# Optimization experiments

Hardware: AMD Instinct MI355X
Metric: run time of the kernel (lower is better)

Reference implementation:

```python
import jax, jax.numpy as jnp
import numpy as np

B, S, H = 1, 4096, 2048
NH, HD = 16, 128
ROPE_N = 32
WINDOW = 1024
EPS = 1e-5


def _build_rope(seq_len, n_elem, base=10000.0):
    theta = 1.0 / (base ** (np.arange(0, n_elem, 2, dtype=np.float32) / n_elem))  # [n_elem/2]
    idx = np.arange(seq_len, dtype=np.float32)
    freqs = np.outer(idx, theta)                     # [S, n_elem/2]
    freqs = np.concatenate([freqs, freqs], axis=-1)  # [S, n_elem]
    return jnp.asarray(np.cos(freqs)), jnp.asarray(np.sin(freqs))


def setup_inputs() -> dict:
    key = jax.random.key(0)
    k1, k2, k3 = jax.random.split(key, 3)
    x = jax.random.normal(k1, (B, S, H), dtype=jnp.float32)
    cos, sin = _build_rope(S, ROPE_N)
    norm_weight = jnp.ones((H,), dtype=jnp.float32)
    qkv_w = jax.random.normal(k2, (3 * H, H), dtype=jnp.float32) * (1.0 / np.sqrt(H))
    o_w = jax.random.normal(k3, (H, H), dtype=jnp.float32) * (1.0 / np.sqrt(H))
    return {"x": x, "cos": cos, "sin": sin, "norm_weight": norm_weight,
            "qkv_w": qkv_w, "o_w": o_w}


def _apply_rope(t, cos, sin):
    # t: [B, NH, S, ROPE_N]; cos/sin: [S, ROPE_N]
    half = t.shape[-1] // 2
    x1, x2 = t[..., :half], t[..., half:]
    rotated = jnp.concatenate([-x2, x1], axis=-1)
    return t * cos + rotated * sin


def reference(x, cos, sin, norm_weight, qkv_w, o_w):
    b, s, h = x.shape
    # RMSNorm (computed in fp32)
    xf = x.astype(jnp.float32)
    ms = jnp.mean(xf * xf, axis=-1, keepdims=True)
    xn = (norm_weight * (xf * jax.lax.rsqrt(ms + EPS))).astype(x.dtype)
    # fused QKV projection
    qkv = jnp.einsum('bsh,oh->bso', xn, qkv_w)  # [B, S, 3H]
    q, k, v = jnp.split(qkv, 3, axis=-1)
    def to_heads(t):
        return t.reshape(b, s, NH, HD).transpose(0, 2, 1, 3)  # [B, NH, S, HD]
    q, k, v = to_heads(q), to_heads(k), to_heads(v)
    # partial RoPE on first ROPE_N dims
    q = jnp.concatenate([_apply_rope(q[..., :ROPE_N], cos, sin), q[..., ROPE_N:]], axis=-1)
    k = jnp.concatenate([_apply_rope(k[..., :ROPE_N], cos, sin), k[..., ROPE_N:]], axis=-1)
    # sliding-window causal attention: query i attends keys j with i-WINDOW <= j <= i
    scale = 1.0 / np.sqrt(HD)
    scores = jnp.einsum('bnqd,bnkd->bnqk', q, k) * scale  # [B, NH, S, S]
    i = jnp.arange(s)[:, None]
    j = jnp.arange(s)[None, :]
    mask = (j <= i) & (j >= i - WINDOW)
    scores = jnp.where(mask, scores, jnp.finfo(scores.dtype).min)
    attn = jax.nn.softmax(scores, axis=-1)
    out = jnp.einsum('bnqk,bnkd->bnqd', attn, v)  # [B, NH, S, HD]
    out = out.transpose(0, 2, 1, 3).reshape(b, s, h)
    return jnp.einsum('bsh,oh->bso', out, o_w)
```

## Files before the change

kernel.cpp:

```cpp
#include <hip/hip_runtime.h>
#include <stdint.h>

#define S_LEN 4096
#define HDIM  2048
#define NHEAD 16
#define HD    128
#define WIN   1024

typedef float  f32x4  __attribute__((ext_vector_type(4)));
typedef float  f32x4v __attribute__((ext_vector_type(4)));
typedef __bf16 bf16x8 __attribute__((ext_vector_type(8)));
typedef short  short8 __attribute__((ext_vector_type(8)));
typedef short  short4v __attribute__((ext_vector_type(4)));

static __device__ __forceinline__ short f2bf(float f) {
  union { float f; uint32_t u; } v; v.f = f;
  uint32_t r = (v.u + 0x7FFFu + ((v.u >> 16) & 1u)) >> 16;
  return (short)(uint16_t)r;
}

static __device__ __forceinline__ void gload_lds16(const void* g, void* l) {
  __builtin_amdgcn_global_load_lds((__attribute__((address_space(1))) void*)g,
                                   (__attribute__((address_space(3))) void*)l,
                                   16, 0, 0);
}

__global__ __launch_bounds__(256) void rmsnorm_k(const float* __restrict__ x,
                                                 const float* __restrict__ w,
                                                 short* __restrict__ xn) {
  const int row = blockIdx.x;
  const int t = threadIdx.x;
  const float* xr = x + (size_t)row * HDIM;
  f32x4v a = *(const f32x4v*)&xr[t * 8];
  f32x4v b = *(const f32x4v*)&xr[t * 8 + 4];
  float ss = a.x*a.x + a.y*a.y + a.z*a.z + a.w*a.w
           + b.x*b.x + b.y*b.y + b.z*b.z + b.w*b.w;
#pragma unroll
  for (int d = 1; d < 64; d <<= 1) ss += __shfl_xor(ss, d, 64);
  __shared__ float sred[4];
  if ((t & 63) == 0) sred[t >> 6] = ss;
  __syncthreads();
  float tot = sred[0] + sred[1] + sred[2] + sred[3];
  float rs = rsqrtf(tot * (1.0f / HDIM) + 1e-5f);
  float vv[8] = {a.x, a.y, a.z, a.w, b.x, b.y, b.z, b.w};
  const float* wp = w + t * 8;
  short8 o;
#pragma unroll
  for (int j = 0; j < 8; ++j) o[j] = f2bf(vv[j] * rs * wp[j]);
  *(short8*)&xn[(size_t)row * HDIM + t * 8] = o;
}

__global__ __launch_bounds__(256) void cvt_k(const float* __restrict__ in,
                                             short* __restrict__ out, int n4) {
  int i = blockIdx.x * 256 + threadIdx.x;
  if (i >= n4) return;
  f32x4v v = *(const f32x4v*)&in[(size_t)i * 4];
  short4v o = { f2bf(v.x), f2bf(v.y), f2bf(v.z), f2bf(v.w) };
  *(short4v*)&out[(size_t)i * 4] = o;
}

template <int EPI>
__global__ __launch_bounds__(512, 2) void gemm_8p(
    const short* __restrict__ A, const short* __restrict__ Bt,
    int M, int N, int K, float* __restrict__ Cf,
    const float* __restrict__ cosb, const float* __restrict__ sinb,
    short* __restrict__ Qo, short* __restrict__ Ko, short* __restrict__ Vt) {
  __shared__ __align__(16) short lds[2][32768];
  const int t = threadIdx.x;
  const int wid = t >> 6, l = t & 63;
  const int lr = l & 15, lg = l >> 4;
  const int wm = wid >> 2, wn = wid & 3;

  int bid = blockIdx.x;
  const int nwg = gridDim.x;
  bid = (bid & 7) * (nwg >> 3) + (bid >> 3);
  const int nby = M >> 8;
  const int by = bid % nby, bx = bid / nby;
  const int brow = by * 256, bcol = bx * 256;

  const int ssl = ((t & 7) ^ ((t >> 3) & 7)) * 8;
  const short* Asrc = A  + (size_t)(brow + (t >> 3)) * K + ssl;
  const short* Bsrc = Bt + (size_t)(bcol + (t >> 3)) * K + ssl;

#define ST_A0(d, kt) do {                                                \
    gload_lds16(Asrc + (size_t)(kt),            &lds[d][t * 8]);         \
    gload_lds16(Asrc + (size_t)64  * K + (kt),  &lds[d][4096 + t * 8]);  } while (0)
#define ST_A1(d, kt) do {                                                \
    gload_lds16(Asrc + (size_t)128 * K + (kt),  &lds[d][8192 + t * 8]);  \
    gload_lds16(Asrc + (size_t)192 * K + (kt),  &lds[d][12288 + t * 8]); } while (0)
#define ST_B0(d, kt) do {                                                \
    gload_lds16(Bsrc + (size_t)(kt),            &lds[d][16384 + t * 8]); \
    gload_lds16(Bsrc + (size_t)64  * K + (kt),  &lds[d][20480 + t * 8]); } while (0)
#define ST_B1(d, kt) do {                                                \
    gload_lds16(Bsrc + (size_t)128 * K + (kt),  &lds[d][24576 + t * 8]); \
    gload_lds16(Bsrc + (size_t)192 * K + (kt),  &lds[d][28672 + t * 8]); } while (0)

  f32x4 acc[8][4] = {};
  const int nt = K >> 6;

  const int s0 = ((lg     ) ^ (lr & 7)) * 8;
  const int s1 = ((lg + 4) ^ (lr & 7)) * 8;
  const int aB = (wm * 128 + lr) * 64;
  const int bB = 16384 + (wn * 64 + lr) * 64;

  ST_A0(0, 0); ST_A1(0, 0); ST_B0(0, 0); ST_B1(0, 0);
  if (nt > 1) { ST_B0(1, 64); ST_A0(1, 64); ST_A1(1, 64); }
  asm volatile("s_waitcnt vmcnt(6)" ::: "memory");
  __builtin_amdgcn_s_barrier();
  __builtin_amdgcn_sched_barrier(0);

  for (int tt = 0; tt < nt; ++tt) {
    const short* P = &lds[tt & 1][0];
    bf16x8 a03[4][2], a47[4][2], b01[2][2], b23[2][2];

#pragma unroll
    for (int m = 0; m < 4; ++m) {
      a03[m][0] = *(const bf16x8*)&P[aB + m * 1024 + s0];
      a03[m][1] = *(const bf16x8*)&P[aB + m * 1024 + s1];
    }
#pragma unroll
    for (int n = 0; n < 2; ++n) {
      b01[n][0] = *(const bf16x8*)&P[bB + n * 1024 + s0];
      b01[n][1] = *(const bf16x8*)&P[bB + n * 1024 + s1];
    }
    if (tt + 1 < nt) ST_B1((tt & 1) ^ 1, (tt + 1) << 6);
    __builtin_amdgcn_s_setprio(1);
#pragma unroll
    for (int m = 0; m < 4; ++m)
#pragma unroll
      for (int n = 0; n < 2; ++n) {
        acc[m][n] = __builtin_amdgcn_mfma_f32_16x16x32_bf16(a03[m][0], b01[n][0], acc[m][n], 0, 0, 0);
        acc[m][n] = __builtin_amdgcn_mfma_f32_16x16x32_bf16(a03[m][1], b01[n][1], acc[m][n], 0, 0, 0);
      }
    __builtin_amdgcn_s_setprio(0);

#pragma unroll
    for (int n = 0; n < 2; ++n) {
      b23[n][0] = *(const bf16x8*)&P[bB + (n + 2) * 1024 + s0];
      b23[n][1] = *(const bf16x8*)&P[bB + (n + 2) * 1024 + s1];
    }
    __builtin_amdgcn_s_setprio(1);
#pragma unroll
    for (int m = 0; m < 4; ++m)
#pragma unroll
      for (int n = 0; n < 2; ++n) {
        acc[m][n + 2] = __builtin_amdgcn_mfma_f32_16x16x32_bf16(a03[m][0], b23[n][0], acc[m][n + 2], 0, 0, 0);
        acc[m][n + 2] = __builtin_amdgcn_mfma_f32_16x16x32_bf16(a03[m][1], b23[n][1], acc[m][n + 2], 0, 0, 0);
      }
    __builtin_amdgcn_s_setprio(0);

#pragma unroll
    for (int m = 0; m < 4; ++m) {
      a47[m][0] = *(const bf16x8*)&P[aB + (m + 4) * 1024 + s0];
      a47[m][1] = *(const bf16x8*)&P[aB + (m + 4) * 1024 + s1];
    }
    __builtin_amdgcn_s_setprio(1);
#pragma unroll
    for (int m = 0; m < 4; ++m)
#pragma unroll
      for (int n = 0; n < 2; ++n) {
        acc[m + 4][n + 2] = __builtin_amdgcn_mfma_f32_16x16x32_bf16(a47[m][0], b23[n][0], acc[m + 4][n + 2], 0, 0, 0);
        acc[m + 4][n + 2] = __builtin_amdgcn_mfma_f32_16x16x32_bf16(a47[m][1], b23[n][1], acc[m + 4][n + 2], 0, 0, 0);
      }
    __builtin_amdgcn_s_setprio(0);

    asm volatile("" ::: "memory");
    __builtin_amdgcn_s_barrier();
    __builtin_amdgcn_sched_barrier(0);

    if (tt + 2 < nt) {
      const int k2 = (tt + 2) << 6;
      ST_B0(tt & 1, k2); ST_A0(tt & 1, k2); ST_A1(tt & 1, k2);
    }
    __builtin_amdgcn_s_setprio(1);
#pragma unroll
    for (int m = 0; m < 4; ++m)
#pragma unroll
      for (int n = 0; n < 2; ++n) {
        acc[m + 4][n] = __builtin_amdgcn_mfma_f32_16x16x32_bf16(a47[m][0], b01[n][0], acc[m + 4][n], 0, 0, 0);
        acc[m + 4][n] = __builtin_amdgcn_mfma_f32_16x16x32_bf16(a47[m][1], b01[n][1], acc[m + 4][n], 0, 0, 0);
      }
    __builtin_amdgcn_s_setprio(0);
    if (tt + 2 < nt) asm volatile("s_waitcnt vmcnt(6)" ::: "memory");
    else             asm volatile("s_waitcnt vmcnt(0)" ::: "memory");
    __builtin_amdgcn_s_barrier();
    __builtin_amdgcn_sched_barrier(0);
  }
#undef ST_A0
#undef ST_A1
#undef ST_B0
#undef ST_B1

  const int row0 = brow + wm * 128, col0 = bcol + wn * 64;
  if (EPI == 0) {
#pragma unroll
    for (int m = 0; m < 8; ++m)
#pragma unroll
      for (int n = 0; n < 4; ++n)
#pragma unroll
        for (int r = 0; r < 4; ++r)
          Cf[(size_t)(row0 + m * 16 + lg * 4 + r) * N + col0 + n * 16 + lr] = acc[m][n][r];
  } else {
    const int sec = col0 >> 11;
    const int headc = (col0 & 2047) >> 7;
    const bool rope = (sec < 2) && ((col0 & 127) == 0);
#pragma unroll
    for (int m = 0; m < 8; ++m) {
#pragma unroll
      for (int r = 0; r < 4; ++r) {
        const int s = row0 + m * 16 + lg * 4 + r;
        float v0 = acc[m][0][r], v1 = acc[m][1][r];
        float v2 = acc[m][2][r], v3 = acc[m][3][r];
        if (rope) {
          const int d0 = lr;
          float c0 = cosb[s * 32 + d0],      sn0 = sinb[s * 32 + d0];
          float c1 = cosb[s * 32 + d0 + 16], sn1 = sinb[s * 32 + d0 + 16];
          float t0 = v0 * c0 - v1 * sn0;
          float t1 = v1 * c1 + v0 * sn1;
          v0 = t0; v1 = t1;
        }
        float vv[4] = {v0, v1, v2, v3};
#pragma unroll
        for (int n = 0; n < 4; ++n) {
          const int col = col0 + n * 16 + lr;
          const int d = col & 127;
          if (sec == 0)
            Qo[((size_t)headc * S_LEN + s) * HD + d] = f2bf(vv[n] * 0.08838834764831845f);
          else if (sec == 1)
            Ko[((size_t)headc * S_LEN + s) * HD + d] = f2bf(vv[n]);
          else
            Vt[((size_t)headc * HD + d) * S_LEN + s] = f2bf(vv[n]);
        }
      }
    }
  }
}

__global__ __launch_bounds__(256) void attn_k(const short* __restrict__ Q,
                                              const short* __restrict__ Kk,
                                              const short* __restrict__ Vt,
                                              short* __restrict__ Ao) {
  __shared__ __align__(16) short Kl[64 * HD];
  __shared__ __align__(16) short Vl[HD * 64];
  __shared__ __align__(16) short Pl[4][16 * 72];
  const int head = blockIdx.y;
  int bxx = blockIdx.x;
  bxx = ((bxx & 7) << 3) | (bxx >> 3);
  const int qb = bxx * 64;
  const int w = threadIdx.x >> 6, l = threadIdx.x & 63;
  const int lr = l & 15, lg = l >> 4;
  const int q0w = qb + w * 16;
  const short* Qh = Q  + (size_t)head * S_LEN * HD;
  const short* Kh = Kk + (size_t)head * S_LEN * HD;
  const short* Vh = Vt + (size_t)head * HD * S_LEN;

  bf16x8 qf[4];
#pragma unroll
  for (int kk = 0; kk < 4; ++kk)
    qf[kk] = *(const bf16x8*)&Qh[(size_t)(q0w + lr) * HD + kk * 32 + lg * 8];

  f32x4 oacc[8] = {};
  float mrow[4], lrow[4];
#pragma unroll
  for (int r = 0; r < 4; ++r) { mrow[r] = -1e30f; lrow[r] = 0.0f; }

  const int k_begin = (qb >= WIN) ? (qb - WIN) : 0;
  const int nt = (qb + 64 - k_begin) >> 6;
  const int swz = (lr & 7) << 4;

  for (int tkv = 0; tkv < nt; ++tkv) {
    const int k0 = k_begin + tkv * 64;
#pragma unroll
    for (int i = 0; i < 4; ++i) {
      const int row = i * 16 + w * 4 + (l >> 4);
      gload_lds16(Kh + (size_t)(k0 + row) * HD + (((l & 15) ^ (row & 7)) * 8),
                  &Kl[(i * 16 + w * 4) * HD]);
    }
#pragma unroll
    for (int i = 0; i < 4; ++i) {
      const int row = i * 32 + w * 8 + (l >> 3);
      gload_lds16(Vh + (size_t)row * S_LEN + k0 + (((l & 7) ^ (row & 7)) * 8),
                  &Vl[(i * 32 + w * 8) * 64]);
    }
    __syncthreads();

    f32x4 sacc[4] = {};
#pragma unroll
    for (int nf = 0; nf < 4; ++nf) {
      const char* kb = (const char*)Kl + (nf * 16 + lr) * 256;
      bf16x8 kf[4];
#pragma unroll
      for (int kk = 0; kk < 4; ++kk)
        kf[kk] = *(const bf16x8*)(kb + ((kk * 64 + lg * 16) ^ swz));
#pragma unroll
      for (int kk = 0; kk < 4; ++kk)
        sacc[nf] = __builtin_amdgcn_mfma_f32_16x16x32_bf16(qf[kk], kf[kk], sacc[nf], 0, 0, 0);
    }

    const bool full = (k0 + 63 <= q0w) && (k0 >= q0w + 15 - WIN);
    float scl[4];
#pragma unroll
    for (int r = 0; r < 4; ++r) {
      const int i = q0w + lg * 4 + r;
      float sv[4];
#pragma unroll
      for (int nf = 0; nf < 4; ++nf) sv[nf] = sacc[nf][r];
      if (!full) {
#pragma unroll
        for (int nf = 0; nf < 4; ++nf) {
          const int j = k0 + nf * 16 + lr;
          if (!((j <= i) && (j + WIN >= i))) sv[nf] = -1e30f;
        }
      }
      float mx = fmaxf(fmaxf(sv[0], sv[1]), fmaxf(sv[2], sv[3]));
#pragma unroll
      for (int d = 1; d < 16; d <<= 1) mx = fmaxf(mx, __shfl_xor(mx, d, 64));
      const float mn = fmaxf(mrow[r], mx);
      const float sc = __expf(mrow[r] - mn);
      mrow[r] = mn;
      float p[4], rs = 0.0f;
#pragma unroll
      for (int nf = 0; nf < 4; ++nf) { p[nf] = __expf(sv[nf] - mn); rs += p[nf]; }
#pragma unroll
      for (int d = 1; d < 16; d <<= 1) rs += __shfl_xor(rs, d, 64);
      lrow[r] = lrow[r] * sc + rs;
      scl[r] = sc;
#pragma unroll
      for (int nf = 0; nf < 4; ++nf)
        Pl[w][(lg * 4 + r) * 72 + nf * 16 + lr] = f2bf(p[nf]);
    }
#pragma unroll
    for (int df = 0; df < 8; ++df)
#pragma unroll
      for (int r = 0; r < 4; ++r) oacc[df][r] *= scl[r];

    bf16x8 pa[2];
#pragma unroll
    for (int kk2 = 0; kk2 < 2; ++kk2)
      pa[kk2] = *(const bf16x8*)&Pl[w][lr * 72 + kk2 * 32 + lg * 8];

#pragma unroll
    for (int df = 0; df < 8; ++df) {
      const char* vb = (const char*)Vl + (df * 16 + lr) * 128;
#pragma unroll
      for (int kk2 = 0; kk2 < 2; ++kk2) {
        bf16x8 vfrag = *(const bf16x8*)(vb + ((kk2 * 64 + lg * 16) ^ swz));
        oacc[df] = __builtin_amdgcn_mfma_f32_16x16x32_bf16(pa[kk2], vfrag, oacc[df], 0, 0, 0);
      }
    }
    __syncthreads();
  }

  float inv[4];
#pragma unroll
  for (int r = 0; r < 4; ++r) inv[r] = 1.0f / lrow[r];
#pragma unroll
  for (int df = 0; df < 8; ++df)
#pragma unroll
    for (int r = 0; r < 4; ++r) {
      const int s = q0w + lg * 4 + r;
      Ao[(size_t)s * HDIM + head * HD + df * 16 + lr] = f2bf(oacc[df][r] * inv[r]);
    }
}

extern "C" void kernel_launch(void* const* d_in, const int* in_sizes, int n_in,
                              void* d_out, int out_size, void* d_ws, size_t ws_size,
                              hipStream_t stream) {
  const float* x    = (const float*)d_in[0];
  const float* cosb = (const float*)d_in[1];
  const float* sinb = (const float*)d_in[2];
  const float* nw   = (const float*)d_in[3];
  const float* qkvw = (const float*)d_in[4];
  const float* ow   = (const float*)d_in[5];
  float* out = (float*)d_out;

  short* ws = (short*)d_ws;
  short* xn = ws;
  short* wb = xn + (size_t)S_LEN * HDIM;
  short* Qb = wb + (size_t)3 * HDIM * HDIM;
  short* Kb = Qb + (size_t)NHEAD * S_LEN * HD;
  short* Vb = Kb + (size_t)NHEAD * S_LEN * HD;
  short* Ao = xn;

  rmsnorm_k<<<S_LEN, 256, 0, stream>>>(x, nw, xn);
  cvt_k<<<(3 * HDIM * HDIM / 4 + 255) / 256, 256, 0, stream>>>(qkvw, wb, 3 * HDIM * HDIM / 4);
  gemm_8p<1><<<(S_LEN / 256) * (3 * HDIM / 256), 512, 0, stream>>>(
      xn, wb, S_LEN, 3 * HDIM, HDIM, nullptr, cosb, sinb, Qb, Kb, Vb);
  cvt_k<<<(HDIM * HDIM / 4 + 255) / 256, 256, 0, stream>>>(ow, wb, HDIM * HDIM / 4);
  attn_k<<<dim3(S_LEN / 64, NHEAD), 256, 0, stream>>>(Qb, Kb, Vb, Ao);
  gemm_8p<0><<<(S_LEN / 256) * (HDIM / 256), 512, 0, stream>>>(
      Ao, wb, S_LEN, HDIM, HDIM, out, nullptr, nullptr, nullptr, nullptr, nullptr);
}
```

Before: 337.0 us.

## Interleave GEMM global loads with MFMA phases using per-phase barriers

Restructures the bf16 GEMM main loop into barrier-separated phases. Each LDS fragment read is followed by an explicit lgkmcnt(0) wait before its MFMA block. Global-to-LDS loads for the next stages are spread across phases: B half 0 is issued as soon as its fragments are consumed, and A afterward. The aim is to overlap memory traffic with compute and keep waves in lockstep, at the cost of several extra workgroup barriers per k-tile.

```diff
diff --git a/kernel.cpp b/kernel.cpp
--- a/kernel.cpp
+++ b/kernel.cpp
@@ -82,18 +82,22 @@
   const short* Asrc = A  + (size_t)(brow + (t >> 3)) * K + ssl;
   const short* Bsrc = Bt + (size_t)(bcol + (t >> 3)) * K + ssl;
 
-#define ST_A0(d, kt) do {                                                \
-    gload_lds16(Asrc + (size_t)(kt),            &lds[d][t * 8]);         \
-    gload_lds16(Asrc + (size_t)64  * K + (kt),  &lds[d][4096 + t * 8]);  } while (0)
-#define ST_A1(d, kt) do {                                                \
-    gload_lds16(Asrc + (size_t)128 * K + (kt),  &lds[d][8192 + t * 8]);  \
-    gload_lds16(Asrc + (size_t)192 * K + (kt),  &lds[d][12288 + t * 8]); } while (0)
-#define ST_B0(d, kt) do {                                                \
-    gload_lds16(Bsrc + (size_t)(kt),            &lds[d][16384 + t * 8]); \
-    gload_lds16(Bsrc + (size_t)64  * K + (kt),  &lds[d][20480 + t * 8]); } while (0)
-#define ST_B1(d, kt) do {                                                \
-    gload_lds16(Bsrc + (size_t)128 * K + (kt),  &lds[d][24576 + t * 8]); \
-    gload_lds16(Bsrc + (size_t)192 * K + (kt),  &lds[d][28672 + t * 8]); } while (0)
+#define ST_A(d, kt, half) do {                                                  \
+    gload_lds16(Asrc + (size_t)((half) * 128     ) * K + (kt),                  \
+                &lds[d][(half) * 8192 + t * 8]);                                \
+    gload_lds16(Asrc + (size_t)((half) * 128 + 64) * K + (kt),                  \
+                &lds[d][(half) * 8192 + 4096 + t * 8]);                         \
+  } while (0)
+#define ST_B(d, kt, half) do {                                                  \
+    gload_lds16(Bsrc + (size_t)((half) * 128     ) * K + (kt),                  \
+                &lds[d][16384 + (half) * 8192 + t * 8]);                        \
+    gload_lds16(Bsrc + (size_t)((half) * 128 + 64) * K + (kt),                  \
+                &lds[d][16384 + (half) * 8192 + 4096 + t * 8]);                 \
+  } while (0)
+
+#define BAR_SCHED  __builtin_amdgcn_s_barrier(); __builtin_amdgcn_sched_barrier(0)
+#define LGKM0      asm volatile("s_waitcnt lgkmcnt(0)" ::: "memory");           \
+                   __builtin_amdgcn_sched_barrier(0)
 
   f32x4 acc[8][4] = {};
   const int nt = K >> 6;
@@ -103,14 +107,15 @@
   const int aB = (wm * 128 + lr) * 64;
   const int bB = 16384 + (wn * 64 + lr) * 64;
 
-  ST_A0(0, 0); ST_A1(0, 0); ST_B0(0, 0); ST_B1(0, 0);
-  if (nt > 1) { ST_B0(1, 64); ST_A0(1, 64); ST_A1(1, 64); }
-  asm volatile("s_waitcnt vmcnt(6)" ::: "memory");
-  __builtin_amdgcn_s_barrier();
-  __builtin_amdgcn_sched_barrier(0);
-
-  for (int tt = 0; tt < nt; ++tt) {
-    const short* P = &lds[tt & 1][0];
+  ST_A(0, 0, 0); ST_A(0, 0, 1); ST_B(0, 0, 0); ST_B(0, 0, 1);
+  if (nt > 1) { ST_A(1, 64, 0); ST_A(1, 64, 1); ST_B(1, 64, 0); }
+  if (nt > 1) asm volatile("s_waitcnt vmcnt(6)" ::: "memory");
+  else        asm volatile("s_waitcnt vmcnt(0)" ::: "memory");
+  BAR_SCHED;
+
+  for (int kt = 0; kt < nt; ++kt) {
+    const int d = kt & 1;
+    const short* P = &lds[d][0];
     bf16x8 a03[4][2], a47[4][2], b01[2][2], b23[2][2];
 
 #pragma unroll
@@ -123,7 +128,9 @@
       b01[n][0] = *(const bf16x8*)&P[bB + n * 1024 + s0];
       b01[n][1] = *(const bf16x8*)&P[bB + n * 1024 + s1];
     }
-    if (tt + 1 < nt) ST_B1((tt & 1) ^ 1, (tt + 1) << 6);
+    if (kt + 1 < nt) ST_B(d ^ 1, (kt + 1) << 6, 1);
+    BAR_SCHED;
+    LGKM0;
     __builtin_amdgcn_s_setprio(1);
 #pragma unroll
     for (int m = 0; m < 4; ++m)
@@ -133,12 +140,15 @@
         acc[m][n] = __builtin_amdgcn_mfma_f32_16x16x32_bf16(a03[m][1], b01[n][1], acc[m][n], 0, 0, 0);
       }
     __builtin_amdgcn_s_setprio(0);
+    BAR_SCHED;
 
 #pragma unroll
     for (int n = 0; n < 2; ++n) {
       b23[n][0] = *(const bf16x8*)&P[bB + (n + 2) * 1024 + s0];
       b23[n][1] = *(const bf16x8*)&P[bB + (n + 2) * 1024 + s1];
     }
+    BAR_SCHED;
+    LGKM0;
     __builtin_amdgcn_s_setprio(1);
 #pragma unroll
     for (int m = 0; m < 4; ++m)
@@ -148,12 +158,16 @@
         acc[m][n + 2] = __builtin_amdgcn_mfma_f32_16x16x32_bf16(a03[m][1], b23[n][1], acc[m][n + 2], 0, 0, 0);
       }
     __builtin_amdgcn_s_setprio(0);
+    BAR_SCHED;
 
 #pragma unroll
     for (int m = 0; m < 4; ++m) {
       a47[m][0] = *(const bf16x8*)&P[aB + (m + 4) * 1024 + s0];
       a47[m][1] = *(const bf16x8*)&P[aB + (m + 4) * 1024 + s1];
     }
+    if (kt + 2 < nt) ST_B(d, (kt + 2) << 6, 0);
+    BAR_SCHED;
+    LGKM0;
     __builtin_amdgcn_s_setprio(1);
 #pragma unroll
     for (int m = 0; m < 4; ++m)
@@ -163,15 +177,10 @@
         acc[m + 4][n + 2] = __builtin_amdgcn_mfma_f32_16x16x32_bf16(a47[m][1], b23[n][1], acc[m + 4][n + 2], 0, 0, 0);
       }
     __builtin_amdgcn_s_setprio(0);
-
-    asm volatile("" ::: "memory");
-    __builtin_amdgcn_s_barrier();
-    __builtin_amdgcn_sched_barrier(0);
-
-    if (tt + 2 < nt) {
-      const int k2 = (tt + 2) << 6;
-      ST_B0(tt & 1, k2); ST_A0(tt & 1, k2); ST_A1(tt & 1, k2);
-    }
+    BAR_SCHED;
+
+    if (kt + 2 < nt) { ST_A(d, (kt + 2) << 6, 0); ST_A(d, (kt + 2) << 6, 1); }
+    BAR_SCHED;
     __builtin_amdgcn_s_setprio(1);
 #pragma unroll
     for (int m = 0; m < 4; ++m)
@@ -181,15 +190,14 @@
         acc[m + 4][n] = __builtin_amdgcn_mfma_f32_16x16x32_bf16(a47[m][1], b01[n][1], acc[m + 4][n], 0, 0, 0);
       }
     __builtin_amdgcn_s_setprio(0);
-    if (tt + 2 < nt) asm volatile("s_waitcnt vmcnt(6)" ::: "memory");
-    else             asm volatile("s_waitcnt vmcnt(0)" ::: "memory");
-    __builtin_amdgcn_s_barrier();
-    __builtin_amdgcn_sched_barrier(0);
+    if (kt + 2 < nt)      asm volatile("s_waitcnt vmcnt(6)" ::: "memory");
+    else if (kt + 1 < nt) asm volatile("s_waitcnt vmcnt(0)" ::: "memory");
+    BAR_SCHED;
   }
-#undef ST_A0
-#undef ST_A1
-#undef ST_B0
-#undef ST_B1
+#undef ST_A
+#undef ST_B
+#undef BAR_SCHED
+#undef LGKM0
 
   const int row0 = brow + wm * 128, col0 = bcol + wn * 64;
   if (EPI == 0) {
```

Result: slower. 351.0 us (+4.2%).
